# Kernel optimization log

Hardware: AMD Instinct MI355X
Metric: run time of the kernel (lower is better)

Reference implementation:

```python
import jax, jax.numpy as jnp
import numpy as np

EMB = 128
SQRT_EMB = 128 ** 0.5
LOGIT_CLIP = 10.0


def setup_inputs() -> dict:
    key = jax.random.key(0)
    ks = jax.random.split(key, 10)
    B, N, M, D = 128, 512, 512, EMB
    s = 1.0 / np.sqrt(D)
    return {
        "encoded_last_node": jax.random.normal(ks[0], (B, N, D), jnp.float32),
        "load": jax.random.uniform(ks[1], (B, N), jnp.float32),
        "cur_dist": jax.random.uniform(ks[2], (B, N, M), jnp.float32),
        "log_scale": jnp.ones((), jnp.float32),
        "ninf_mask": jnp.zeros((B, N, M), jnp.float32),
        "encoded_nodes": jax.random.normal(ks[3], (B, M, D), jnp.float32),
        "Wq_last": jax.random.normal(ks[4], (D, D + 1), jnp.float32) * s,
        "Wk": jax.random.normal(ks[5], (D, D), jnp.float32) * s,
        "Wv": jax.random.normal(ks[6], (D, D), jnp.float32) * s,
        "alpha1": jnp.ones((1,), jnp.float32),
        "alpha2": jnp.ones((1,), jnp.float32),
    }


def reference(encoded_last_node, load, cur_dist, log_scale, ninf_mask,
              encoded_nodes, Wq_last, Wk, Wv, alpha1, alpha2):
    # set_kv
    k = jnp.einsum('bmd,ed->bme', encoded_nodes, Wk)   # (B,M,D)
    v = jnp.einsum('bmd,ed->bme', encoded_nodes, Wv)   # (B,M,D)
    # query from last node + load
    input_cat = jnp.concatenate([encoded_last_node, load[:, :, None]], axis=2)  # (B,N,D+1)
    q = jnp.einsum('bnc,ec->bne', input_cat, Wq_last)  # (B,N,D)
    # AAFM: exp-bias linear attention with sigmoid gate
    adaptation_bias = -alpha1[0] * log_scale * cur_dist + ninf_mask  # (B,N,M)
    eb = jnp.exp(adaptation_bias)
    ek = jnp.exp(k)
    num = jnp.einsum('bnm,bmd->bnd', eb, ek * v)
    den = jnp.einsum('bnm,bmd->bnd', eb, ek)
    weighted = jnp.nan_to_num(num / den)  # mirrors torch nan_to_num correction
    aafm_out = jax.nn.sigmoid(q) * weighted  # (B,N,D)
    # single-head decode score against encoder embeddings
    score = jnp.einsum('bnd,bmd->bnm', aafm_out, encoded_nodes)
    score_scaled = score / SQRT_EMB - alpha2[0] * log_scale * cur_dist
    score_masked = LOGIT_CLIP * jnp.tanh(score_scaled) + ninf_mask
    probs = jax.nn.softmax(score_masked, axis=-1)
    return probs
```

## Files before the change

### kernel.cpp

```cpp
#include <hip/hip_runtime.h>
#include <math.h>

#define B 128
#define N 512
#define M 512
#define D 128

typedef __attribute__((ext_vector_type(8))) short s16x8;
typedef __attribute__((ext_vector_type(4))) short s16x4;
typedef __attribute__((ext_vector_type(4))) float f32x4;

#define MFMA16(a, b, c) __builtin_amdgcn_mfma_f32_16x16x32_bf16(a, b, c, 0, 0, 0)

__device__ __forceinline__ void gload16(const void* g, void* l) {
    __builtin_amdgcn_global_load_lds(
        (const __attribute__((address_space(1))) unsigned int*)g,
        (__attribute__((address_space(3))) unsigned int*)l, 16, 0, 0);
}

__device__ __forceinline__ float fast_tanh(float x) {
    x = fminf(fmaxf(x, -15.f), 15.f);
    float E = __expf(2.f * x);
    return 1.f - 2.f / (E + 1.f);
}

__device__ __forceinline__ unsigned short bf16rne(float x) {
    unsigned u = __float_as_uint(x);
    return (unsigned short)((u + 0x7FFF + ((u >> 16) & 1)) >> 16);
}

__device__ __forceinline__ void fsplit(float x, short& h, short& l) {
    unsigned u = __float_as_uint(x);
    h = (short)(u >> 16);
    float fh = __uint_as_float(u & 0xffff0000u);
    l = (short)(__float_as_uint(x - fh) >> 16);
}

__device__ __forceinline__ void fsplit8(float4 x0, float4 x1, s16x8& h, s16x8& l) {
    short a, b;
    fsplit(x0.x, a, b); h[0] = a; l[0] = b;
    fsplit(x0.y, a, b); h[1] = a; l[1] = b;
    fsplit(x0.z, a, b); h[2] = a; l[2] = b;
    fsplit(x0.w, a, b); h[3] = a; l[3] = b;
    fsplit(x1.x, a, b); h[4] = a; l[4] = b;
    fsplit(x1.y, a, b); h[5] = a; l[5] = b;
    fsplit(x1.z, a, b); h[6] = a; l[6] = b;
    fsplit(x1.w, a, b); h[7] = a; l[7] = b;
}

__device__ __forceinline__ void ebsplit(float4 c0, float4 c1, float4 f0, float4 f1,
                                        float a1ls, s16x8& ah, s16x8& al) {
    float4 e0, e1;
    e0.x = __expf(fmaf(-a1ls, c0.x, f0.x));
    e0.y = __expf(fmaf(-a1ls, c0.y, f0.y));
    e0.z = __expf(fmaf(-a1ls, c0.z, f0.z));
    e0.w = __expf(fmaf(-a1ls, c0.w, f0.w));
    e1.x = __expf(fmaf(-a1ls, c1.x, f1.x));
    e1.y = __expf(fmaf(-a1ls, c1.y, f1.y));
    e1.z = __expf(fmaf(-a1ls, c1.z, f1.z));
    e1.w = __expf(fmaf(-a1ls, c1.w, f1.w));
    fsplit8(e0, e1, ah, al);
}

__global__ void k_prep_w(const float* __restrict__ Wk, const float* __restrict__ Wv,
                         const float* __restrict__ Wq,
                         unsigned short* __restrict__ Wk_hi, unsigned short* __restrict__ Wk_lo,
                         unsigned short* __restrict__ Wv_hi, unsigned short* __restrict__ Wv_lo,
                         unsigned short* __restrict__ Wq_hi, unsigned short* __restrict__ Wq_lo) {
    int i = blockIdx.x * 256 + threadIdx.x;
    short h, l;
    if (i < 16384) {
        fsplit(Wk[i], h, l); Wk_hi[i] = (unsigned short)h; Wk_lo[i] = (unsigned short)l;
    } else if (i < 32768) {
        int j = i - 16384;
        fsplit(Wv[j], h, l); Wv_hi[j] = (unsigned short)h; Wv_lo[j] = (unsigned short)l;
    } else {
        int j = i - 32768; int e = j >> 7, d = j & 127;
        fsplit(Wq[e * 129 + d], h, l); Wq_hi[j] = (unsigned short)h; Wq_lo[j] = (unsigned short)l;
    }
}

__global__ __launch_bounds__(256) void k_kv(const float* __restrict__ enc,
        const unsigned short* __restrict__ Wk_hi, const unsigned short* __restrict__ Wk_lo,
        const unsigned short* __restrict__ Wv_hi, const unsigned short* __restrict__ Wv_lo,
        unsigned short* __restrict__ EKb, unsigned short* __restrict__ EKVb) {
    int b = blockIdx.y;
    int wave = threadIdx.x >> 6, lane = threadIdx.x & 63;
    int row = lane & 15, kg = lane >> 4;
    int m0 = blockIdx.x * 64 + wave * 16;
    f32x4 acc[16];
#pragma unroll
    for (int i = 0; i < 16; i++) acc[i] = (f32x4)0.f;
    const float* ap = enc + ((size_t)b * M + m0 + row) * D + kg * 8;
#pragma unroll
    for (int ks = 0; ks < 4; ks++) {
        float4 x0 = *(const float4*)(ap + ks * 32);
        float4 x1 = *(const float4*)(ap + ks * 32 + 4);
        s16x8 ah, al;
        fsplit8(x0, x1, ah, al);
        int wb = ks * 32 + kg * 8;
#pragma unroll
        for (int ct = 0; ct < 8; ct++) {
            int e = ct * 16 + row;
            s16x8 bh = *(const s16x8*)(Wk_hi + e * D + wb);
            s16x8 bl = *(const s16x8*)(Wk_lo + e * D + wb);
            acc[ct] = MFMA16(ah, bh, acc[ct]);
            acc[ct] = MFMA16(al, bh, acc[ct]);
            acc[ct] = MFMA16(ah, bl, acc[ct]);
            bh = *(const s16x8*)(Wv_hi + e * D + wb);
            bl = *(const s16x8*)(Wv_lo + e * D + wb);
            acc[8 + ct] = MFMA16(ah, bh, acc[8 + ct]);
            acc[8 + ct] = MFMA16(al, bh, acc[8 + ct]);
            acc[8 + ct] = MFMA16(ah, bl, acc[8 + ct]);
        }
    }
#pragma unroll
    for (int ct = 0; ct < 8; ct++) {
        int e = ct * 16 + row;
        s16x4 kb, vb;
#pragma unroll
        for (int r = 0; r < 4; r++) {
            float ek = __expf(acc[ct][r]);
            float ev = ek * acc[8 + ct][r];
            kb[r] = (short)bf16rne(ek);
            vb[r] = (short)bf16rne(ev);
        }
        int m = m0 + kg * 4;
        int chunk = (m & 31) >> 3;
        int p = chunk ^ (e & 3);
        size_t o = ((size_t)b * D + e) * M + (size_t)(m & ~31) + p * 8 + (m & 7);
        *(s16x4*)(EKb + o) = kb;
        *(s16x4*)(EKVb + o) = vb;
    }
}

__global__ __launch_bounds__(256) void k_q(const float* __restrict__ encl,
        const float* __restrict__ loadv, const float* __restrict__ Wq,
        const unsigned short* __restrict__ Wq_hi, const unsigned short* __restrict__ Wq_lo,
        float* __restrict__ SQ) {
    int b = blockIdx.y;
    int wave = threadIdx.x >> 6, lane = threadIdx.x & 63;
    int row = lane & 15, kg = lane >> 4;
    int n0 = blockIdx.x * 64 + wave * 16;
    f32x4 acc[8];
#pragma unroll
    for (int i = 0; i < 8; i++) acc[i] = (f32x4)0.f;
    const float* ap = encl + ((size_t)b * N + n0 + row) * D + kg * 8;
#pragma unroll
    for (int ks = 0; ks < 4; ks++) {
        float4 x0 = *(const float4*)(ap + ks * 32);
        float4 x1 = *(const float4*)(ap + ks * 32 + 4);
        s16x8 ah, al;
        fsplit8(x0, x1, ah, al);
        int wb = ks * 32 + kg * 8;
#pragma unroll
        for (int ct = 0; ct < 8; ct++) {
            int e = ct * 16 + row;
            s16x8 bh = *(const s16x8*)(Wq_hi + e * D + wb);
            s16x8 bl = *(const s16x8*)(Wq_lo + e * D + wb);
            acc[ct] = MFMA16(ah, bh, acc[ct]);
            acc[ct] = MFMA16(al, bh, acc[ct]);
            acc[ct] = MFMA16(ah, bl, acc[ct]);
        }
    }
#pragma unroll
    for (int r = 0; r < 4; r++) {
        int n = n0 + kg * 4 + r;
        float lv = loadv[(size_t)b * N + n];
        size_t ro = ((size_t)b * N + n) * D;
#pragma unroll
        for (int ct = 0; ct < 8; ct++) {
            int e = ct * 16 + row;
            float q = acc[ct][r] + lv * Wq[e * 129 + 128];
            SQ[ro + e] = 1.f / (1.f + __expf(-q));
        }
    }
}

__global__ __launch_bounds__(256) void k_numden(
        const float* __restrict__ cd, const float* __restrict__ ninf,
        const unsigned short* __restrict__ EKVb, const unsigned short* __restrict__ EKb,
        float* __restrict__ SQ,
        const float* __restrict__ a1p, const float* __restrict__ lsp) {
    int o = blockIdx.x;
    int xcd = o & 7, j = o >> 3;
    int b = ((j >> 3) << 3) + xcd;
    int nb = j & 7;
    int w = threadIdx.x >> 6, lane = threadIdx.x & 63;
    int ns = w >> 1, eh = w & 1;
    int row = lane & 15, kg = lane >> 4;
    int n0 = nb * 64 + ns * 32;
    __shared__ __align__(16) char lds[2][16384];
    float a1ls = a1p[0] * lsp[0];
    const char* gEKV = (const char*)EKVb + (size_t)b * D * M * 2;
    const char* gEK  = (const char*)EKb  + (size_t)b * D * M * 2;
    f32x4 accN[2][4], accD[2][4];
#pragma unroll
    for (int s = 0; s < 2; s++)
#pragma unroll
        for (int i = 0; i < 4; i++) { accN[s][i] = (f32x4)0.f; accD[s][i] = (f32x4)0.f; }
    const float* cdp0 = cd + ((size_t)b * N + n0 + row) * M + kg * 8;
    const float* nfp0 = ninf + ((size_t)b * N + n0 + row) * M + kg * 8;
    const float* cdp1 = cdp0 + (size_t)16 * M;
    const float* nfp1 = nfp0 + (size_t)16 * M;
    int rbase = eh * 4096 + row * 64 + ((kg ^ (row & 3)) << 4);

#define STAGE_ND(buf, mt)                                                        \
    _Pragma("unroll")                                                            \
    for (int jv = 0; jv < 4; jv++) {                                             \
        int idx = jv * 256 + threadIdx.x;                                        \
        const char* gb = (idx >> 9) ? gEK : gEKV;                                \
        int rem = idx & 511;                                                     \
        gload16(gb + (size_t)(rem >> 2) * 1024 + (mt) * 64 + (rem & 3) * 16,     \
                (char*)lds + (buf) * 16384 + idx * 16);                          \
    }

    float4 c00 = *(const float4*)(cdp0), c01 = *(const float4*)(cdp0 + 4);
    float4 f00 = *(const float4*)(nfp0), f01 = *(const float4*)(nfp0 + 4);
    float4 c10 = *(const float4*)(cdp1), c11 = *(const float4*)(cdp1 + 4);
    float4 f10 = *(const float4*)(nfp1), f11 = *(const float4*)(nfp1 + 4);
    STAGE_ND(0, 0)

#pragma unroll 2
    for (int mt = 0; mt < 16; mt++) {
        int cur = mt & 1;
        __syncthreads();
        s16x8 ah0, al0, ah1, al1;
        ebsplit(c00, c01, f00, f01, a1ls, ah0, al0);
        ebsplit(c10, c11, f10, f11, a1ls, ah1, al1);
        if (mt < 15) {
            int m = (mt + 1) * 32;
            c00 = *(const float4*)(cdp0 + m); c01 = *(const float4*)(cdp0 + m + 4);
            f00 = *(const float4*)(nfp0 + m); f01 = *(const float4*)(nfp0 + m + 4);
            c10 = *(const float4*)(cdp1 + m); c11 = *(const float4*)(cdp1 + m + 4);
            f10 = *(const float4*)(nfp1 + m); f11 = *(const float4*)(nfp1 + m + 4);
            STAGE_ND(cur ^ 1, mt + 1)
        }
        const char* L = (const char*)lds + cur * 16384;
#pragma unroll
        for (int ct = 0; ct < 4; ct++) {
            int ro = ct * 1024 + rbase;
            s16x8 bv = *(const s16x8*)(L + ro);
            s16x8 bk = *(const s16x8*)(L + 8192 + ro);
            accN[0][ct] = MFMA16(ah0, bv, accN[0][ct]);
            accN[0][ct] = MFMA16(al0, bv, accN[0][ct]);
            accN[1][ct] = MFMA16(ah1, bv, accN[1][ct]);
            accN[1][ct] = MFMA16(al1, bv, accN[1][ct]);
            accD[0][ct] = MFMA16(ah0, bk, accD[0][ct]);
            accD[0][ct] = MFMA16(al0, bk, accD[0][ct]);
            accD[1][ct] = MFMA16(ah1, bk, accD[1][ct]);
            accD[1][ct] = MFMA16(al1, bk, accD[1][ct]);
        }
    }
#pragma unroll
    for (int s = 0; s < 2; s++) {
#pragma unroll
        for (int r = 0; r < 4; r++) {
            int n = n0 + s * 16 + kg * 4 + r;
            size_t ro = ((size_t)b * N + n) * D;
#pragma unroll
            for (int ct = 0; ct < 4; ct++) {
                int e = eh * 64 + ct * 16 + row;
                float num = accN[s][ct][r], den = accD[s][ct][r];
                float ww = (den != 0.f) ? num / den : 0.f;
                float aafm = SQ[ro + e] * ww;
                unsigned u = __float_as_uint(aafm);
                unsigned hi = u >> 16;
                float fh = __uint_as_float(u & 0xffff0000u);
                unsigned lo = __float_as_uint(aafm - fh) >> 16;
                SQ[ro + e] = __uint_as_float(hi | (lo << 16));
            }
        }
    }
}

__global__ void k_encsplit(const float* __restrict__ enc,
                           unsigned short* __restrict__ Eh, unsigned short* __restrict__ El) {
    size_t i = (size_t)blockIdx.x * 256 + threadIdx.x;
    size_t bm = i >> 4;
    int c = (int)(i & 15);
    int m = (int)(bm & 511);
    int p = c ^ (m & 7);
    const float* src = enc + bm * 128 + c * 8;
    float4 x0 = *(const float4*)(src);
    float4 x1 = *(const float4*)(src + 4);
    s16x8 h, l;
    fsplit8(x0, x1, h, l);
    *(s16x8*)(Eh + bm * 128 + p * 8) = h;
    *(s16x8*)(El + bm * 128 + p * 8) = l;
}

__global__ __launch_bounds__(256) void k_score(
        const float* __restrict__ AAFM,
        const unsigned short* __restrict__ Eh, const unsigned short* __restrict__ El,
        const float* __restrict__ cd, const float* __restrict__ ninf,
        const float* __restrict__ a2p, const float* __restrict__ lsp,
        float* __restrict__ out) {
    int o = blockIdx.x;
    int xcd = o & 7, j = o >> 3;
    int b = ((j >> 4) << 3) + xcd;
    int nb = j & 15;
    int n0 = nb * 32;
    int w = threadIdx.x >> 6, lane = threadIdx.x & 63;
    int row = lane & 15, kg = lane >> 4;
    int ng = w >> 1, mh = w & 1;
    __shared__ __align__(16) char lds[2][16384];
    __shared__ float redm[32][2];
    __shared__ float reds[32][2];
    float a2ls = a2p[0] * lsp[0];
    const float invs = 0.08838834764831845f;

    const float* apk = AAFM + ((size_t)b * N + n0 + ng * 16 + row) * D + kg * 8;
    s16x8 ah[4], al[4];
#pragma unroll
    for (int es = 0; es < 4; es++) {
        float4 w0 = *(const float4*)(apk + es * 32);
        float4 w1 = *(const float4*)(apk + es * 32 + 4);
        unsigned u;
        u = __float_as_uint(w0.x); ah[es][0] = (short)(u & 0xffff); al[es][0] = (short)(u >> 16);
        u = __float_as_uint(w0.y); ah[es][1] = (short)(u & 0xffff); al[es][1] = (short)(u >> 16);
        u = __float_as_uint(w0.z); ah[es][2] = (short)(u & 0xffff); al[es][2] = (short)(u >> 16);
        u = __float_as_uint(w0.w); ah[es][3] = (short)(u & 0xffff); al[es][3] = (short)(u >> 16);
        u = __float_as_uint(w1.x); ah[es][4] = (short)(u & 0xffff); al[es][4] = (short)(u >> 16);
        u = __float_as_uint(w1.y); ah[es][5] = (short)(u & 0xffff); al[es][5] = (short)(u >> 16);
        u = __float_as_uint(w1.z); ah[es][6] = (short)(u & 0xffff); al[es][6] = (short)(u >> 16);
        u = __float_as_uint(w1.w); ah[es][7] = (short)(u & 0xffff); al[es][7] = (short)(u >> 16);
    }
    f32x4 acc[16];
#pragma unroll
    for (int i = 0; i < 16; i++) acc[i] = (f32x4)0.f;

#define STAGE_SC(buf, mc)                                                          \
    _Pragma("unroll")                                                              \
    for (int jv = 0; jv < 4; jv++) {                                               \
        int id = (w * 4 + jv) * 64 + lane;                                         \
        int arr = id >> 9, rem = id & 511;                                         \
        const unsigned short* gb = arr ? El : Eh;                                  \
        gload16((const char*)gb + ((size_t)b * M + (mc) * 32) * 256 + rem * 16,    \
                (char*)lds + (buf) * 16384 + arr * 8192 + rem * 16);               \
    }

    STAGE_SC(0, 0)
#pragma unroll
    for (int mc = 0; mc < 16; mc++) {
        int cur = mc & 1;
        __syncthreads();
        int mloc = mh * 16 + row;
        int rbase = mloc * 256;
        int sw = mloc & 7;
        const char* L = (const char*)lds + cur * 16384;
#pragma unroll
        for (int es = 0; es < 4; es++) {
            int ph = (4 * es + kg) ^ sw;
            s16x8 bh = *(const s16x8*)(L + rbase + ph * 16);
            s16x8 bl = *(const s16x8*)(L + 8192 + rbase + ph * 16);
            acc[mc] = MFMA16(ah[es], bh, acc[mc]);
            acc[mc] = MFMA16(al[es], bh, acc[mc]);
            acc[mc] = MFMA16(ah[es], bl, acc[mc]);
        }
        float cdv[4], nfv[4];
#pragma unroll
        for (int r = 0; r < 4; r++) {
            size_t idx = ((size_t)b * N + n0 + ng * 16 + kg * 4 + r) * M
                       + (size_t)mc * 32 + mloc;
            cdv[r] = cd[idx];
            nfv[r] = ninf[idx];
        }
        if (mc < 15) STAGE_SC(cur ^ 1, mc + 1)
#pragma unroll
        for (int r = 0; r < 4; r++) {
            acc[mc][r] = 10.f * fast_tanh(fmaf(acc[mc][r], invs, -a2ls * cdv[r]))
                       + nfv[r];
        }
    }
    float mx[4], sm[4];
#pragma unroll
    for (int r = 0; r < 4; r++) {
        float m = acc[0][r];
#pragma unroll
        for (int a = 1; a < 16; a++) m = fmaxf(m, acc[a][r]);
#pragma unroll
        for (int s = 1; s < 16; s <<= 1) m = fmaxf(m, __shfl_xor(m, s, 64));
        mx[r] = m;
    }
    int rl = ng * 16 + kg * 4;
    if (row == 0) {
#pragma unroll
        for (int r = 0; r < 4; r++) redm[rl + r][mh] = mx[r];
    }
    __syncthreads();
#pragma unroll
    for (int r = 0; r < 4; r++) {
        float m = fmaxf(redm[rl + r][0], redm[rl + r][1]);
        float s = 0.f;
#pragma unroll
        for (int a = 0; a < 16; a++) {
            float e = __expf(acc[a][r] - m);
            acc[a][r] = e;
            s += e;
        }
#pragma unroll
        for (int sh = 1; sh < 16; sh <<= 1) s += __shfl_xor(s, sh, 64);
        sm[r] = s;
    }
    if (row == 0) {
#pragma unroll
        for (int r = 0; r < 4; r++) reds[rl + r][mh] = sm[r];
    }
    __syncthreads();
#pragma unroll
    for (int r = 0; r < 4; r++) {
        float inv = 1.f / (reds[rl + r][0] + reds[rl + r][1]);
        size_t ro = ((size_t)b * N + n0 + rl + r) * M;
#pragma unroll
        for (int a = 0; a < 16; a++) {
            out[ro + a * 32 + mh * 16 + row] = acc[a][r] * inv;
        }
    }
}

extern "C" void kernel_launch(void* const* d_in, const int* in_sizes, int n_in,
                              void* d_out, int out_size, void* d_ws, size_t ws_size,
                              hipStream_t stream) {
    const float* encl  = (const float*)d_in[0];
    const float* loadv = (const float*)d_in[1];
    const float* cdist = (const float*)d_in[2];
    const float* ls    = (const float*)d_in[3];
    const float* ninf  = (const float*)d_in[4];
    const float* enc   = (const float*)d_in[5];
    const float* Wq    = (const float*)d_in[6];
    const float* Wk    = (const float*)d_in[7];
    const float* Wv    = (const float*)d_in[8];
    const float* a1    = (const float*)d_in[9];
    const float* a2    = (const float*)d_in[10];
    char* ws = (char*)d_ws;
    unsigned short* EKb     = (unsigned short*)(ws);
    unsigned short* EKVb    = (unsigned short*)(ws + 33554432);
    float*          SQ      = (float*)(ws + 67108864);
    unsigned short* Wk_hi   = (unsigned short*)(ws + 100663296);
    unsigned short* Wk_lo   = (unsigned short*)(ws + 100663296 + 32768);
    unsigned short* Wv_hi   = (unsigned short*)(ws + 100663296 + 65536);
    unsigned short* Wv_lo   = (unsigned short*)(ws + 100663296 + 98304);
    unsigned short* Wq_hi   = (unsigned short*)(ws + 100663296 + 131072);
    unsigned short* Wq_lo   = (unsigned short*)(ws + 100663296 + 163840);
    unsigned short* ENC_hi  = EKb;
    unsigned short* ENC_lo  = EKVb;
    float* out = (float*)d_out;

    k_prep_w<<<192, 256, 0, stream>>>(Wk, Wv, Wq, Wk_hi, Wk_lo, Wv_hi, Wv_lo, Wq_hi, Wq_lo);
    k_kv<<<dim3(8, 128), 256, 0, stream>>>(enc, Wk_hi, Wk_lo, Wv_hi, Wv_lo, EKb, EKVb);
    k_q<<<dim3(8, 128), 256, 0, stream>>>(encl, loadv, Wq, Wq_hi, Wq_lo, SQ);
    k_numden<<<1024, 256, 0, stream>>>(cdist, ninf, EKVb, EKb, SQ, a1, ls);
    k_encsplit<<<4096, 256, 0, stream>>>(enc, ENC_hi, ENC_lo);
    k_score<<<2048, 256, 0, stream>>>(SQ, ENC_hi, ENC_lo, cdist, ninf, a2, ls, out);
}
```

Before: 369.3 us.

## Triple-buffer LDS staging with explicit vmcnt waits in numden and score kernels

Both the num/den kernel and the score kernel move from double-buffered to triple-buffered LDS staging, keeping two tiles in flight. Each iteration waits with a hand-set s_waitcnt vmcnt and one raw barrier instead of a full __syncthreads. The cur_dist and ninf_mask loads are now issued one iteration ahead into separate registers, and k_score hoists its per-row index math out of the loop. Launch bounds now request 3 blocks per SIMD group to hide more memory latency. The cost is more LDS per block (48KB) and extra register pressure, which could cause spills or reduce occupancy, and the hand-counted vmcnt values must match the exact load order the compiler emits.

```diff
diff --git a/kernel.cpp b/kernel.cpp
--- a/kernel.cpp
+++ b/kernel.cpp
@@ -11,6 +11,10 @@
 typedef __attribute__((ext_vector_type(4))) float f32x4;
 
 #define MFMA16(a, b, c) __builtin_amdgcn_mfma_f32_16x16x32_bf16(a, b, c, 0, 0, 0)
+
+#define VMCNT4()  asm volatile("s_waitcnt vmcnt(4)" ::: "memory")
+#define VMCNT8()  asm volatile("s_waitcnt vmcnt(8)" ::: "memory")
+#define VMCNT12() asm volatile("s_waitcnt vmcnt(12)" ::: "memory")
 
 __device__ __forceinline__ void gload16(const void* g, void* l) {
     __builtin_amdgcn_global_load_lds(
@@ -177,7 +181,7 @@
     }
 }
 
-__global__ __launch_bounds__(256) void k_numden(
+__global__ __launch_bounds__(256, 3) void k_numden(
         const float* __restrict__ cd, const float* __restrict__ ninf,
         const unsigned short* __restrict__ EKVb, const unsigned short* __restrict__ EKb,
         float* __restrict__ SQ,
@@ -190,7 +194,7 @@
     int ns = w >> 1, eh = w & 1;
     int row = lane & 15, kg = lane >> 4;
     int n0 = nb * 64 + ns * 32;
-    __shared__ __align__(16) char lds[2][16384];
+    __shared__ __align__(16) char lds[3][16384];
     float a1ls = a1p[0] * lsp[0];
     const char* gEKV = (const char*)EKVb + (size_t)b * D * M * 2;
     const char* gEK  = (const char*)EKb  + (size_t)b * D * M * 2;
@@ -205,38 +209,41 @@
     const float* nfp1 = nfp0 + (size_t)16 * M;
     int rbase = eh * 4096 + row * 64 + ((kg ^ (row & 3)) << 4);
 
-#define STAGE_ND(buf, mt)                                                        \
+#define STAGE_ND(ldsbase, mt)                                                    \
     _Pragma("unroll")                                                            \
     for (int jv = 0; jv < 4; jv++) {                                             \
         int idx = jv * 256 + threadIdx.x;                                        \
         const char* gb = (idx >> 9) ? gEK : gEKV;                                \
         int rem = idx & 511;                                                     \
-        gload16(gb + (size_t)(rem >> 2) * 1024 + (mt) * 64 + (rem & 3) * 16,     \
-                (char*)lds + (buf) * 16384 + idx * 16);                          \
+        gload16(gb + (size_t)(rem >> 2) * 1024 + (size_t)(mt) * 64 + (rem & 3) * 16, \
+                (char*)(ldsbase) + idx * 16);                                    \
     }
 
     float4 c00 = *(const float4*)(cdp0), c01 = *(const float4*)(cdp0 + 4);
     float4 f00 = *(const float4*)(nfp0), f01 = *(const float4*)(nfp0 + 4);
     float4 c10 = *(const float4*)(cdp1), c11 = *(const float4*)(cdp1 + 4);
     float4 f10 = *(const float4*)(nfp1), f11 = *(const float4*)(nfp1 + 4);
-    STAGE_ND(0, 0)
-
-#pragma unroll 2
+    STAGE_ND((char*)lds, 0)
+    STAGE_ND((char*)lds + 16384, 1)
+
+#pragma unroll
     for (int mt = 0; mt < 16; mt++) {
-        int cur = mt & 1;
-        __syncthreads();
+        if (mt == 0) { VMCNT4(); } else if (mt == 15) { VMCNT8(); } else { VMCNT12(); }
+        __builtin_amdgcn_s_barrier();
+        __builtin_amdgcn_sched_barrier(0);
+        float4 nc00, nc01, nf00, nf01, nc10, nc11, nf10, nf11;
+        if (mt < 15) {
+            int m = (mt + 1) * 32;
+            nc00 = *(const float4*)(cdp0 + m); nc01 = *(const float4*)(cdp0 + m + 4);
+            nf00 = *(const float4*)(nfp0 + m); nf01 = *(const float4*)(nfp0 + m + 4);
+            nc10 = *(const float4*)(cdp1 + m); nc11 = *(const float4*)(cdp1 + m + 4);
+            nf10 = *(const float4*)(nfp1 + m); nf11 = *(const float4*)(nfp1 + m + 4);
+        }
+        if (mt < 14) STAGE_ND((char*)lds + ((mt + 2) % 3) * 16384, mt + 2)
         s16x8 ah0, al0, ah1, al1;
         ebsplit(c00, c01, f00, f01, a1ls, ah0, al0);
         ebsplit(c10, c11, f10, f11, a1ls, ah1, al1);
-        if (mt < 15) {
-            int m = (mt + 1) * 32;
-            c00 = *(const float4*)(cdp0 + m); c01 = *(const float4*)(cdp0 + m + 4);
-            f00 = *(const float4*)(nfp0 + m); f01 = *(const float4*)(nfp0 + m + 4);
-            c10 = *(const float4*)(cdp1 + m); c11 = *(const float4*)(cdp1 + m + 4);
-            f10 = *(const float4*)(nfp1 + m); f11 = *(const float4*)(nfp1 + m + 4);
-            STAGE_ND(cur ^ 1, mt + 1)
-        }
-        const char* L = (const char*)lds + cur * 16384;
+        const char* L = (const char*)lds + (mt % 3) * 16384;
 #pragma unroll
         for (int ct = 0; ct < 4; ct++) {
             int ro = ct * 1024 + rbase;
@@ -250,6 +257,10 @@
             accD[0][ct] = MFMA16(al0, bk, accD[0][ct]);
             accD[1][ct] = MFMA16(ah1, bk, accD[1][ct]);
             accD[1][ct] = MFMA16(al1, bk, accD[1][ct]);
+        }
+        if (mt < 15) {
+            c00 = nc00; c01 = nc01; f00 = nf00; f01 = nf01;
+            c10 = nc10; c11 = nc11; f10 = nf10; f11 = nf11;
         }
     }
 #pragma unroll
@@ -290,7 +301,7 @@
     *(s16x8*)(El + bm * 128 + p * 8) = l;
 }
 
-__global__ __launch_bounds__(256) void k_score(
+__global__ __launch_bounds__(256, 3) void k_score(
         const float* __restrict__ AAFM,
         const unsigned short* __restrict__ Eh, const unsigned short* __restrict__ El,
         const float* __restrict__ cd, const float* __restrict__ ninf,
@@ -304,7 +315,7 @@
     int w = threadIdx.x >> 6, lane = threadIdx.x & 63;
     int row = lane & 15, kg = lane >> 4;
     int ng = w >> 1, mh = w & 1;
-    __shared__ __align__(16) char lds[2][16384];
+    __shared__ __align__(16) char lds[3][16384];
     __shared__ float redm[32][2];
     __shared__ float reds[32][2];
     float a2ls = a2p[0] * lsp[0];
@@ -330,25 +341,48 @@
 #pragma unroll
     for (int i = 0; i < 16; i++) acc[i] = (f32x4)0.f;
 
-#define STAGE_SC(buf, mc)                                                          \
+    int mloc = mh * 16 + row;
+    int rbase = mloc * 256;
+    int sw = mloc & 7;
+    size_t rowidx[4];
+#pragma unroll
+    for (int r = 0; r < 4; r++)
+        rowidx[r] = ((size_t)b * N + n0 + ng * 16 + kg * 4 + r) * M;
+
+#define STAGE_SC(ldsbase, mc)                                                      \
     _Pragma("unroll")                                                              \
     for (int jv = 0; jv < 4; jv++) {                                               \
         int id = (w * 4 + jv) * 64 + lane;                                         \
         int arr = id >> 9, rem = id & 511;                                         \
         const unsigned short* gb = arr ? El : Eh;                                  \
-        gload16((const char*)gb + ((size_t)b * M + (mc) * 32) * 256 + rem * 16,    \
-                (char*)lds + (buf) * 16384 + arr * 8192 + rem * 16);               \
-    }
-
-    STAGE_SC(0, 0)
+        gload16((const char*)gb + ((size_t)b * M + (size_t)(mc) * 32) * 256 + rem * 16, \
+                (char*)(ldsbase) + arr * 8192 + rem * 16);                         \
+    }
+
+    float cdv[4], nfv[4];
+#pragma unroll
+    for (int r = 0; r < 4; r++) {
+        cdv[r] = cd[rowidx[r] + mloc];
+        nfv[r] = ninf[rowidx[r] + mloc];
+    }
+    STAGE_SC((char*)lds, 0)
+    STAGE_SC((char*)lds + 16384, 1)
+
 #pragma unroll
     for (int mc = 0; mc < 16; mc++) {
-        int cur = mc & 1;
-        __syncthreads();
-        int mloc = mh * 16 + row;
-        int rbase = mloc * 256;
-        int sw = mloc & 7;
-        const char* L = (const char*)lds + cur * 16384;
+        if (mc == 0) { VMCNT4(); } else if (mc == 15) { VMCNT8(); } else { VMCNT12(); }
+        __builtin_amdgcn_s_barrier();
+        __builtin_amdgcn_sched_barrier(0);
+        float ncd[4], nnf[4];
+        if (mc < 15) {
+#pragma unroll
+            for (int r = 0; r < 4; r++) {
+                ncd[r] = cd[rowidx[r] + (size_t)(mc + 1) * 32 + mloc];
+                nnf[r] = ninf[rowidx[r] + (size_t)(mc + 1) * 32 + mloc];
+            }
+        }
+        if (mc < 14) STAGE_SC((char*)lds + ((mc + 2) % 3) * 16384, mc + 2)
+        const char* L = (const char*)lds + (mc % 3) * 16384;
 #pragma unroll
         for (int es = 0; es < 4; es++) {
             int ph = (4 * es + kg) ^ sw;
@@ -358,19 +392,14 @@
             acc[mc] = MFMA16(al[es], bh, acc[mc]);
             acc[mc] = MFMA16(ah[es], bl, acc[mc]);
         }
-        float cdv[4], nfv[4];
-#pragma unroll
-        for (int r = 0; r < 4; r++) {
-            size_t idx = ((size_t)b * N + n0 + ng * 16 + kg * 4 + r) * M
-                       + (size_t)mc * 32 + mloc;
-            cdv[r] = cd[idx];
-            nfv[r] = ninf[idx];
-        }
-        if (mc < 15) STAGE_SC(cur ^ 1, mc + 1)
 #pragma unroll
         for (int r = 0; r < 4; r++) {
             acc[mc][r] = 10.f * fast_tanh(fmaf(acc[mc][r], invs, -a2ls * cdv[r]))
                        + nfv[r];
+        }
+        if (mc < 15) {
+#pragma unroll
+            for (int r = 0; r < 4; r++) { cdv[r] = ncd[r]; nfv[r] = nnf[r]; }
         }
     }
     float mx[4], sm[4];
```

Result: faster. 358.3 us (-3.0%).

## Fuse query projection, num/den attention, and score softmax into one kernel

Applied to the files above, without the earlier changes.

Merges k_q, k_numden and k_score into a single kernel per 32-row block. The query sigmoid and the aafm output now stay in registers and LDS instead of going through a global SQ buffer. The exp-bias operand is also packed as a single bf16 instead of a hi/lo split, which halves the num/den MFMAs but lowers precision. The cost is that cur_dist and ninf_mask are now read twice per block at smaller tiles, the num/den stage is recomputed at a different block granularity, and register pressure rises under launch_bounds(256,3).

```diff
diff --git a/kernel.cpp b/kernel.cpp
--- a/kernel.cpp
+++ b/kernel.cpp
@@ -48,18 +48,16 @@
     fsplit(x1.w, a, b); h[7] = a; l[7] = b;
 }
 
-__device__ __forceinline__ void ebsplit(float4 c0, float4 c1, float4 f0, float4 f1,
-                                        float a1ls, s16x8& ah, s16x8& al) {
-    float4 e0, e1;
-    e0.x = __expf(fmaf(-a1ls, c0.x, f0.x));
-    e0.y = __expf(fmaf(-a1ls, c0.y, f0.y));
-    e0.z = __expf(fmaf(-a1ls, c0.z, f0.z));
-    e0.w = __expf(fmaf(-a1ls, c0.w, f0.w));
-    e1.x = __expf(fmaf(-a1ls, c1.x, f1.x));
-    e1.y = __expf(fmaf(-a1ls, c1.y, f1.y));
-    e1.z = __expf(fmaf(-a1ls, c1.z, f1.z));
-    e1.w = __expf(fmaf(-a1ls, c1.w, f1.w));
-    fsplit8(e0, e1, ah, al);
+__device__ __forceinline__ void ebpack(float4 c0, float4 c1, float4 f0, float4 f1,
+                                       float a1ls, s16x8& a) {
+    a[0] = (short)bf16rne(__expf(fmaf(-a1ls, c0.x, f0.x)));
+    a[1] = (short)bf16rne(__expf(fmaf(-a1ls, c0.y, f0.y)));
+    a[2] = (short)bf16rne(__expf(fmaf(-a1ls, c0.z, f0.z)));
+    a[3] = (short)bf16rne(__expf(fmaf(-a1ls, c0.w, f0.w)));
+    a[4] = (short)bf16rne(__expf(fmaf(-a1ls, c1.x, f1.x)));
+    a[5] = (short)bf16rne(__expf(fmaf(-a1ls, c1.y, f1.y)));
+    a[6] = (short)bf16rne(__expf(fmaf(-a1ls, c1.z, f1.z)));
+    a[7] = (short)bf16rne(__expf(fmaf(-a1ls, c1.w, f1.w)));
 }
 
 __global__ void k_prep_w(const float* __restrict__ Wk, const float* __restrict__ Wv,
@@ -134,146 +132,6 @@
     }
 }
 
-__global__ __launch_bounds__(256) void k_q(const float* __restrict__ encl,
-        const float* __restrict__ loadv, const float* __restrict__ Wq,
-        const unsigned short* __restrict__ Wq_hi, const unsigned short* __restrict__ Wq_lo,
-        float* __restrict__ SQ) {
-    int b = blockIdx.y;
-    int wave = threadIdx.x >> 6, lane = threadIdx.x & 63;
-    int row = lane & 15, kg = lane >> 4;
-    int n0 = blockIdx.x * 64 + wave * 16;
-    f32x4 acc[8];
-#pragma unroll
-    for (int i = 0; i < 8; i++) acc[i] = (f32x4)0.f;
-    const float* ap = encl + ((size_t)b * N + n0 + row) * D + kg * 8;
-#pragma unroll
-    for (int ks = 0; ks < 4; ks++) {
-        float4 x0 = *(const float4*)(ap + ks * 32);
-        float4 x1 = *(const float4*)(ap + ks * 32 + 4);
-        s16x8 ah, al;
-        fsplit8(x0, x1, ah, al);
-        int wb = ks * 32 + kg * 8;
-#pragma unroll
-        for (int ct = 0; ct < 8; ct++) {
-            int e = ct * 16 + row;
-            s16x8 bh = *(const s16x8*)(Wq_hi + e * D + wb);
-            s16x8 bl = *(const s16x8*)(Wq_lo + e * D + wb);
-            acc[ct] = MFMA16(ah, bh, acc[ct]);
-            acc[ct] = MFMA16(al, bh, acc[ct]);
-            acc[ct] = MFMA16(ah, bl, acc[ct]);
-        }
-    }
-#pragma unroll
-    for (int r = 0; r < 4; r++) {
-        int n = n0 + kg * 4 + r;
-        float lv = loadv[(size_t)b * N + n];
-        size_t ro = ((size_t)b * N + n) * D;
-#pragma unroll
-        for (int ct = 0; ct < 8; ct++) {
-            int e = ct * 16 + row;
-            float q = acc[ct][r] + lv * Wq[e * 129 + 128];
-            SQ[ro + e] = 1.f / (1.f + __expf(-q));
-        }
-    }
-}
-
-__global__ __launch_bounds__(256) void k_numden(
-        const float* __restrict__ cd, const float* __restrict__ ninf,
-        const unsigned short* __restrict__ EKVb, const unsigned short* __restrict__ EKb,
-        float* __restrict__ SQ,
-        const float* __restrict__ a1p, const float* __restrict__ lsp) {
-    int o = blockIdx.x;
-    int xcd = o & 7, j = o >> 3;
-    int b = ((j >> 3) << 3) + xcd;
-    int nb = j & 7;
-    int w = threadIdx.x >> 6, lane = threadIdx.x & 63;
-    int ns = w >> 1, eh = w & 1;
-    int row = lane & 15, kg = lane >> 4;
-    int n0 = nb * 64 + ns * 32;
-    __shared__ __align__(16) char lds[2][16384];
-    float a1ls = a1p[0] * lsp[0];
-    const char* gEKV = (const char*)EKVb + (size_t)b * D * M * 2;
-    const char* gEK  = (const char*)EKb  + (size_t)b * D * M * 2;
-    f32x4 accN[2][4], accD[2][4];
-#pragma unroll
-    for (int s = 0; s < 2; s++)
-#pragma unroll
-        for (int i = 0; i < 4; i++) { accN[s][i] = (f32x4)0.f; accD[s][i] = (f32x4)0.f; }
-    const float* cdp0 = cd + ((size_t)b * N + n0 + row) * M + kg * 8;
-    const float* nfp0 = ninf + ((size_t)b * N + n0 + row) * M + kg * 8;
-    const float* cdp1 = cdp0 + (size_t)16 * M;
-    const float* nfp1 = nfp0 + (size_t)16 * M;
-    int rbase = eh * 4096 + row * 64 + ((kg ^ (row & 3)) << 4);
-
-#define STAGE_ND(buf, mt)                                                        \
-    _Pragma("unroll")                                                            \
-    for (int jv = 0; jv < 4; jv++) {                                             \
-        int idx = jv * 256 + threadIdx.x;                                        \
-        const char* gb = (idx >> 9) ? gEK : gEKV;                                \
-        int rem = idx & 511;                                                     \
-        gload16(gb + (size_t)(rem >> 2) * 1024 + (mt) * 64 + (rem & 3) * 16,     \
-                (char*)lds + (buf) * 16384 + idx * 16);                          \
-    }
-
-    float4 c00 = *(const float4*)(cdp0), c01 = *(const float4*)(cdp0 + 4);
-    float4 f00 = *(const float4*)(nfp0), f01 = *(const float4*)(nfp0 + 4);
-    float4 c10 = *(const float4*)(cdp1), c11 = *(const float4*)(cdp1 + 4);
-    float4 f10 = *(const float4*)(nfp1), f11 = *(const float4*)(nfp1 + 4);
-    STAGE_ND(0, 0)
-
-#pragma unroll 2
-    for (int mt = 0; mt < 16; mt++) {
-        int cur = mt & 1;
-        __syncthreads();
-        s16x8 ah0, al0, ah1, al1;
-        ebsplit(c00, c01, f00, f01, a1ls, ah0, al0);
-        ebsplit(c10, c11, f10, f11, a1ls, ah1, al1);
-        if (mt < 15) {
-            int m = (mt + 1) * 32;
-            c00 = *(const float4*)(cdp0 + m); c01 = *(const float4*)(cdp0 + m + 4);
-            f00 = *(const float4*)(nfp0 + m); f01 = *(const float4*)(nfp0 + m + 4);
-            c10 = *(const float4*)(cdp1 + m); c11 = *(const float4*)(cdp1 + m + 4);
-            f10 = *(const float4*)(nfp1 + m); f11 = *(const float4*)(nfp1 + m + 4);
-            STAGE_ND(cur ^ 1, mt + 1)
-        }
-        const char* L = (const char*)lds + cur * 16384;
-#pragma unroll
-        for (int ct = 0; ct < 4; ct++) {
-            int ro = ct * 1024 + rbase;
-            s16x8 bv = *(const s16x8*)(L + ro);
-            s16x8 bk = *(const s16x8*)(L + 8192 + ro);
-            accN[0][ct] = MFMA16(ah0, bv, accN[0][ct]);
-            accN[0][ct] = MFMA16(al0, bv, accN[0][ct]);
-            accN[1][ct] = MFMA16(ah1, bv, accN[1][ct]);
-            accN[1][ct] = MFMA16(al1, bv, accN[1][ct]);
-            accD[0][ct] = MFMA16(ah0, bk, accD[0][ct]);
-            accD[0][ct] = MFMA16(al0, bk, accD[0][ct]);
-            accD[1][ct] = MFMA16(ah1, bk, accD[1][ct]);
-            accD[1][ct] = MFMA16(al1, bk, accD[1][ct]);
-        }
-    }
-#pragma unroll
-    for (int s = 0; s < 2; s++) {
-#pragma unroll
-        for (int r = 0; r < 4; r++) {
-            int n = n0 + s * 16 + kg * 4 + r;
-            size_t ro = ((size_t)b * N + n) * D;
-#pragma unroll
-            for (int ct = 0; ct < 4; ct++) {
-                int e = eh * 64 + ct * 16 + row;
-                float num = accN[s][ct][r], den = accD[s][ct][r];
-                float ww = (den != 0.f) ? num / den : 0.f;
-                float aafm = SQ[ro + e] * ww;
-                unsigned u = __float_as_uint(aafm);
-                unsigned hi = u >> 16;
-                float fh = __uint_as_float(u & 0xffff0000u);
-                unsigned lo = __float_as_uint(aafm - fh) >> 16;
-                SQ[ro + e] = __uint_as_float(hi | (lo << 16));
-            }
-        }
-    }
-}
-
 __global__ void k_encsplit(const float* __restrict__ enc,
                            unsigned short* __restrict__ Eh, unsigned short* __restrict__ El) {
     size_t i = (size_t)blockIdx.x * 256 + threadIdx.x;
@@ -290,12 +148,15 @@
     *(s16x8*)(El + bm * 128 + p * 8) = l;
 }
 
-__global__ __launch_bounds__(256) void k_score(
-        const float* __restrict__ AAFM,
+__global__ __launch_bounds__(256, 3) void k_fused(
+        const float* __restrict__ encl, const float* __restrict__ loadv,
+        const float* __restrict__ Wq,
+        const unsigned short* __restrict__ Wq_hi, const unsigned short* __restrict__ Wq_lo,
+        const float* __restrict__ cd, const float* __restrict__ ninf,
+        const unsigned short* __restrict__ EKVb, const unsigned short* __restrict__ EKb,
         const unsigned short* __restrict__ Eh, const unsigned short* __restrict__ El,
-        const float* __restrict__ cd, const float* __restrict__ ninf,
-        const float* __restrict__ a2p, const float* __restrict__ lsp,
-        float* __restrict__ out) {
+        const float* __restrict__ a1p, const float* __restrict__ a2p,
+        const float* __restrict__ lsp, float* __restrict__ out) {
     int o = blockIdx.x;
     int xcd = o & 7, j = o >> 3;
     int b = ((j >> 4) << 3) + xcd;
@@ -305,17 +166,135 @@
     int row = lane & 15, kg = lane >> 4;
     int ng = w >> 1, mh = w & 1;
     __shared__ __align__(16) char lds[2][16384];
-    __shared__ float redm[32][2];
-    __shared__ float reds[32][2];
+    __shared__ float redm[32][2], reds[32][2];
+    float a1ls = a1p[0] * lsp[0];
     float a2ls = a2p[0] * lsp[0];
     const float invs = 0.08838834764831845f;
 
-    const float* apk = AAFM + ((size_t)b * N + n0 + ng * 16 + row) * D + kg * 8;
+    f32x4 sqa[2][2];
+#pragma unroll
+    for (int s = 0; s < 2; s++)
+#pragma unroll
+        for (int ct = 0; ct < 2; ct++) sqa[s][ct] = (f32x4)0.f;
+#pragma unroll
+    for (int s = 0; s < 2; s++) {
+        const float* ap = encl + ((size_t)b * N + n0 + s * 16 + row) * D + kg * 8;
+#pragma unroll
+        for (int ks = 0; ks < 4; ks++) {
+            float4 x0 = *(const float4*)(ap + ks * 32);
+            float4 x1 = *(const float4*)(ap + ks * 32 + 4);
+            s16x8 ah, al;
+            fsplit8(x0, x1, ah, al);
+            int wb = ks * 32 + kg * 8;
+#pragma unroll
+            for (int ct = 0; ct < 2; ct++) {
+                int e = w * 32 + ct * 16 + row;
+                s16x8 bh = *(const s16x8*)(Wq_hi + e * D + wb);
+                s16x8 bl = *(const s16x8*)(Wq_lo + e * D + wb);
+                sqa[s][ct] = MFMA16(ah, bh, sqa[s][ct]);
+                sqa[s][ct] = MFMA16(al, bh, sqa[s][ct]);
+                sqa[s][ct] = MFMA16(ah, bl, sqa[s][ct]);
+            }
+        }
+    }
+    float sqv[2][2][4];
+#pragma unroll
+    for (int s = 0; s < 2; s++)
+#pragma unroll
+        for (int ct = 0; ct < 2; ct++) {
+            int e = w * 32 + ct * 16 + row;
+            float wcol = Wq[e * 129 + 128];
+#pragma unroll
+            for (int r = 0; r < 4; r++) {
+                int n = n0 + s * 16 + kg * 4 + r;
+                float q = sqa[s][ct][r] + loadv[(size_t)b * N + n] * wcol;
+                sqv[s][ct][r] = 1.f / (1.f + __expf(-q));
+            }
+        }
+
+    f32x4 accN[2][2], accD[2][2];
+#pragma unroll
+    for (int s = 0; s < 2; s++)
+#pragma unroll
+        for (int i = 0; i < 2; i++) { accN[s][i] = (f32x4)0.f; accD[s][i] = (f32x4)0.f; }
+    const char* gEKV = (const char*)EKVb + (size_t)b * D * M * 2;
+    const char* gEK  = (const char*)EKb  + (size_t)b * D * M * 2;
+    const float* cdp0 = cd + ((size_t)b * N + n0 + row) * M + kg * 8;
+    const float* nfp0 = ninf + ((size_t)b * N + n0 + row) * M + kg * 8;
+    const float* cdp1 = cdp0 + (size_t)16 * M;
+    const float* nfp1 = nfp0 + (size_t)16 * M;
+    int rbase = w * 2048 + row * 64 + ((kg ^ (row & 3)) << 4);
+
+#define STAGE_ND(ldsbase, mt)                                                    \
+    _Pragma("unroll")                                                            \
+    for (int jv = 0; jv < 4; jv++) {                                             \
+        int idx = jv * 256 + threadIdx.x;                                        \
+        const char* gb = (idx >> 9) ? gEK : gEKV;                                \
+        int rem = idx & 511;                                                     \
+        gload16(gb + (size_t)(rem >> 2) * 1024 + (size_t)(mt) * 64 + (rem & 3) * 16, \
+                (char*)(ldsbase) + idx * 16);                                    \
+    }
+
+    float4 c00 = *(const float4*)(cdp0), c01 = *(const float4*)(cdp0 + 4);
+    float4 f00 = *(const float4*)(nfp0), f01 = *(const float4*)(nfp0 + 4);
+    float4 c10 = *(const float4*)(cdp1), c11 = *(const float4*)(cdp1 + 4);
+    float4 f10 = *(const float4*)(nfp1), f11 = *(const float4*)(nfp1 + 4);
+    STAGE_ND((char*)lds, 0)
+
+#pragma unroll 2
+    for (int mt = 0; mt < 16; mt++) {
+        int cur = mt & 1;
+        __syncthreads();
+        s16x8 a0, a1;
+        ebpack(c00, c01, f00, f01, a1ls, a0);
+        ebpack(c10, c11, f10, f11, a1ls, a1);
+        if (mt < 15) {
+            int m = (mt + 1) * 32;
+            c00 = *(const float4*)(cdp0 + m); c01 = *(const float4*)(cdp0 + m + 4);
+            f00 = *(const float4*)(nfp0 + m); f01 = *(const float4*)(nfp0 + m + 4);
+            c10 = *(const float4*)(cdp1 + m); c11 = *(const float4*)(cdp1 + m + 4);
+            f10 = *(const float4*)(nfp1 + m); f11 = *(const float4*)(nfp1 + m + 4);
+            STAGE_ND((char*)lds + (cur ^ 1) * 16384, mt + 1)
+        }
+        const char* L = (const char*)lds + cur * 16384;
+#pragma unroll
+        for (int ct = 0; ct < 2; ct++) {
+            int ro = ct * 1024 + rbase;
+            s16x8 bv = *(const s16x8*)(L + ro);
+            s16x8 bk = *(const s16x8*)(L + 8192 + ro);
+            accN[0][ct] = MFMA16(a0, bv, accN[0][ct]);
+            accN[1][ct] = MFMA16(a1, bv, accN[1][ct]);
+            accD[0][ct] = MFMA16(a0, bk, accD[0][ct]);
+            accD[1][ct] = MFMA16(a1, bk, accD[1][ct]);
+        }
+    }
+
+    float* af = (float*)lds;
+#pragma unroll
+    for (int s = 0; s < 2; s++)
+#pragma unroll
+        for (int ct = 0; ct < 2; ct++) {
+            int e = w * 32 + ct * 16 + row;
+#pragma unroll
+            for (int r = 0; r < 4; r++) {
+                int nl = s * 16 + kg * 4 + r;
+                float num = accN[s][ct][r], den = accD[s][ct][r];
+                float ww = (den != 0.f) ? num / den : 0.f;
+                float aafm = sqv[s][ct][r] * ww;
+                unsigned u = __float_as_uint(aafm);
+                unsigned hi = u >> 16;
+                float fh = __uint_as_float(u & 0xffff0000u);
+                unsigned lo = __float_as_uint(aafm - fh) >> 16;
+                af[nl * 128 + e] = __uint_as_float(hi | (lo << 16));
+            }
+        }
+    __syncthreads();
     s16x8 ah[4], al[4];
 #pragma unroll
     for (int es = 0; es < 4; es++) {
-        float4 w0 = *(const float4*)(apk + es * 32);
-        float4 w1 = *(const float4*)(apk + es * 32 + 4);
+        const float* src = af + (ng * 16 + row) * 128 + es * 32 + kg * 8;
+        float4 w0 = *(const float4*)(src);
+        float4 w1 = *(const float4*)(src + 4);
         unsigned u;
         u = __float_as_uint(w0.x); ah[es][0] = (short)(u & 0xffff); al[es][0] = (short)(u >> 16);
         u = __float_as_uint(w0.y); ah[es][1] = (short)(u & 0xffff); al[es][1] = (short)(u >> 16);
@@ -326,34 +305,40 @@
         u = __float_as_uint(w1.z); ah[es][6] = (short)(u & 0xffff); al[es][6] = (short)(u >> 16);
         u = __float_as_uint(w1.w); ah[es][7] = (short)(u & 0xffff); al[es][7] = (short)(u >> 16);
     }
+    __syncthreads();
+
     f32x4 acc[16];
 #pragma unroll
     for (int i = 0; i < 16; i++) acc[i] = (f32x4)0.f;
-
-#define STAGE_SC(buf, mc)                                                          \
+    int mloc = mh * 16 + row;
+    int rb2 = mloc * 256;
+    int sw = mloc & 7;
+    size_t rowidx[4];
+#pragma unroll
+    for (int r = 0; r < 4; r++)
+        rowidx[r] = ((size_t)b * N + n0 + ng * 16 + kg * 4 + r) * M;
+
+#define STAGE_SC(ldsbase, mc)                                                      \
     _Pragma("unroll")                                                              \
     for (int jv = 0; jv < 4; jv++) {                                               \
         int id = (w * 4 + jv) * 64 + lane;                                         \
         int arr = id >> 9, rem = id & 511;                                         \
         const unsigned short* gb = arr ? El : Eh;                                  \
-        gload16((const char*)gb + ((size_t)b * M + (mc) * 32) * 256 + rem * 16,    \
-                (char*)lds + (buf) * 16384 + arr * 8192 + rem * 16);               \
-    }
-
-    STAGE_SC(0, 0)
+        gload16((const char*)gb + ((size_t)b * M + (size_t)(mc) * 32) * 256 + rem * 16, \
+                (char*)(ldsbase) + arr * 8192 + rem * 16);                         \
+    }
+
+    STAGE_SC((char*)lds, 0)
 #pragma unroll
     for (int mc = 0; mc < 16; mc++) {
         int cur = mc & 1;
         __syncthreads();
-        int mloc = mh * 16 + row;
-        int rbase = mloc * 256;
-        int sw = mloc & 7;
         const char* L = (const char*)lds + cur * 16384;
 #pragma unroll
         for (int es = 0; es < 4; es++) {
             int ph = (4 * es + kg) ^ sw;
-            s16x8 bh = *(const s16x8*)(L + rbase + ph * 16);
-            s16x8 bl = *(const s16x8*)(L + 8192 + rbase + ph * 16);
+            s16x8 bh = *(const s16x8*)(L + rb2 + ph * 16);
+            s16x8 bl = *(const s16x8*)(L + 8192 + rb2 + ph * 16);
             acc[mc] = MFMA16(ah[es], bh, acc[mc]);
             acc[mc] = MFMA16(al[es], bh, acc[mc]);
             acc[mc] = MFMA16(ah[es], bl, acc[mc]);
@@ -361,12 +346,11 @@
         float cdv[4], nfv[4];
 #pragma unroll
         for (int r = 0; r < 4; r++) {
-            size_t idx = ((size_t)b * N + n0 + ng * 16 + kg * 4 + r) * M
-                       + (size_t)mc * 32 + mloc;
+            size_t idx = rowidx[r] + (size_t)mc * 32 + mloc;
             cdv[r] = cd[idx];
             nfv[r] = ninf[idx];
         }
-        if (mc < 15) STAGE_SC(cur ^ 1, mc + 1)
+        if (mc < 15) STAGE_SC((char*)lds + (cur ^ 1) * 16384, mc + 1)
 #pragma unroll
         for (int r = 0; r < 4; r++) {
             acc[mc][r] = 10.f * fast_tanh(fmaf(acc[mc][r], invs, -a2ls * cdv[r]))
@@ -435,22 +419,21 @@
     const float* a2    = (const float*)d_in[10];
     char* ws = (char*)d_ws;
     unsigned short* EKb     = (unsigned short*)(ws);
-    unsigned short* EKVb    = (unsigned short*)(ws + 33554432);
-    float*          SQ      = (float*)(ws + 67108864);
-    unsigned short* Wk_hi   = (unsigned short*)(ws + 100663296);
-    unsigned short* Wk_lo   = (unsigned short*)(ws + 100663296 + 32768);
-    unsigned short* Wv_hi   = (unsigned short*)(ws + 100663296 + 65536);
-    unsigned short* Wv_lo   = (unsigned short*)(ws + 100663296 + 98304);
-    unsigned short* Wq_hi   = (unsigned short*)(ws + 100663296 + 131072);
-    unsigned short* Wq_lo   = (unsigned short*)(ws + 100663296 + 163840);
-    unsigned short* ENC_hi  = EKb;
-    unsigned short* ENC_lo  = EKVb;
+    unsigned short* EKVb    = (unsigned short*)(ws + 16777216);
+    unsigned short* ENC_hi  = (unsigned short*)(ws + 33554432);
+    unsigned short* ENC_lo  = (unsigned short*)(ws + 50331648);
+    unsigned short* Wk_hi   = (unsigned short*)(ws + 67108864);
+    unsigned short* Wk_lo   = (unsigned short*)(ws + 67108864 + 32768);
+    unsigned short* Wv_hi   = (unsigned short*)(ws + 67108864 + 65536);
+    unsigned short* Wv_lo   = (unsigned short*)(ws + 67108864 + 98304);
+    unsigned short* Wq_hi   = (unsigned short*)(ws + 67108864 + 131072);
+    unsigned short* Wq_lo   = (unsigned short*)(ws + 67108864 + 163840);
     float* out = (float*)d_out;
 
     k_prep_w<<<192, 256, 0, stream>>>(Wk, Wv, Wq, Wk_hi, Wk_lo, Wv_hi, Wv_lo, Wq_hi, Wq_lo);
     k_kv<<<dim3(8, 128), 256, 0, stream>>>(enc, Wk_hi, Wk_lo, Wv_hi, Wv_lo, EKb, EKVb);
-    k_q<<<dim3(8, 128), 256, 0, stream>>>(encl, loadv, Wq, Wq_hi, Wq_lo, SQ);
-    k_numden<<<1024, 256, 0, stream>>>(cdist, ninf, EKVb, EKb, SQ, a1, ls);
     k_encsplit<<<4096, 256, 0, stream>>>(enc, ENC_hi, ENC_lo);
-    k_score<<<2048, 256, 0, stream>>>(SQ, ENC_hi, ENC_lo, cdist, ninf, a2, ls, out);
-}
+    k_fused<<<2048, 256, 0, stream>>>(encl, loadv, Wq, Wq_hi, Wq_lo,
+                                      cdist, ninf, EKVb, EKb, ENC_hi, ENC_lo,
+                                      a1, a2, ls, out);
+}
```

Result: no change. 363.1 us (-1.7%).
